# Kernel optimization log

Measured on AMD Instinct MI355X. Metric: run time of the kernel, lower is better.

## Reference

```python
import jax, jax.numpy as jnp
import numpy as np

B, S, E, H, LD, P, NC = 4, 256, 256, 8, 128, 256, 2
N = S * P  # total points (static)
EPS = 1e-5


def setup_inputs() -> dict:
    key = jax.random.key(0)
    ks = jax.random.split(key, 12)
    r = lambda i, shape, s: jax.random.normal(ks[i], shape, jnp.float32) * s
    return dict(
        gl_feats=jax.random.normal(ks[0], (S, B, E), jnp.float32),
        lo_feats=jax.random.normal(ks[1], (B, N, LD), jnp.float32),
        centroids=jax.random.normal(ks[2], (B, S, 2), jnp.float32),
        np_cluster=jnp.full((S,), P, jnp.int32),
        fc1_w=r(3, (16, 2), 0.5), fc1_b=jnp.zeros(16, jnp.float32),
        fc2_w=r(4, (E, 16), 0.1), fc2_b=jnp.zeros(E, jnp.float32),
        in_proj_w=r(5, (3 * E, E), 0.05), in_proj_b=jnp.zeros(3 * E, jnp.float32),
        out_proj_w=r(6, (E, E), 0.05), out_proj_b=jnp.zeros(E, jnp.float32),
        conv2_w=r(7, (E // 2, LD + E), 0.05), conv2_b=jnp.zeros(E // 2, jnp.float32),
        bn2_gamma=jnp.ones(E // 2, jnp.float32), bn2_beta=jnp.zeros(E // 2, jnp.float32),
        bn2_mean=jnp.zeros(E // 2, jnp.float32), bn2_var=jnp.ones(E // 2, jnp.float32),
        conv3_w=r(8, (64, E // 2), 0.05), conv3_b=jnp.zeros(64, jnp.float32),
        bn3_gamma=jnp.ones(64, jnp.float32), bn3_beta=jnp.zeros(64, jnp.float32),
        bn3_mean=jnp.zeros(64, jnp.float32), bn3_var=jnp.ones(64, jnp.float32),
        conv4_w=r(9, (NC, 64), 0.05), conv4_b=jnp.zeros(NC, jnp.float32),
    )


def _bn(z, g, b, m, v):
    # inference-mode BatchNorm1d over the channel (last) axis
    return (z - m) * jax.lax.rsqrt(v + EPS) * g + b


def reference(gl_feats, lo_feats, centroids, np_cluster,
              fc1_w, fc1_b, fc2_w, fc2_b,
              in_proj_w, in_proj_b, out_proj_w, out_proj_b,
              conv2_w, conv2_b, bn2_gamma, bn2_beta, bn2_mean, bn2_var,
              conv3_w, conv3_b, bn3_gamma, bn3_beta, bn3_mean, bn3_var,
              conv4_w, conv4_b):
    # positional encoding of centroids: Linear(2,16) -> leaky_relu -> Linear(16,E)
    h = centroids @ fc1_w.T + fc1_b                      # [B,S,16]
    h = jnp.where(h >= 0, h, 0.01 * h)                   # leaky_relu_, slope 0.01
    pos = h @ fc2_w.T + fc2_b                            # [B,S,E]
    x = gl_feats.transpose(1, 0, 2) + pos                # [B,S,E] (torch MHA is seq-first)

    # MultiheadAttention (self-attn, eval-mode dropout=identity)
    qkv = x @ in_proj_w.T + in_proj_b                    # [B,S,3E]
    q, k, v = jnp.split(qkv, 3, axis=-1)
    dh = E // H
    qh = q.reshape(B, S, H, dh)
    kh = k.reshape(B, S, H, dh)
    vh = v.reshape(B, S, H, dh)
    scores = jnp.einsum('bqhd,bkhd->bhqk', qh, kh) * (1.0 / np.sqrt(dh))
    attn = jax.nn.softmax(scores, axis=-1)               # [B,H,S,S]
    ctx = jnp.einsum('bhqk,bkhd->bqhd', attn, vh).reshape(B, S, E)
    attn_out = ctx @ out_proj_w.T + out_proj_b           # [B,S,E]

    # segment-broadcast: replace the python repeat/cat loop with a gather
    cluster_ids = jnp.repeat(jnp.arange(S), np_cluster, total_repeat_length=N)  # [N]
    global_feat = attn_out[:, cluster_ids, :]            # [B,N,E]

    pc = jnp.concatenate([lo_feats, global_feat], axis=2)  # [B,N,LD+E]
    # 1x1 Conv1d == pointwise Linear over channels
    h2 = jax.nn.relu(_bn(pc @ conv2_w.T + conv2_b, bn2_gamma, bn2_beta, bn2_mean, bn2_var))
    h3 = jax.nn.relu(_bn(h2 @ conv3_w.T + conv3_b, bn3_gamma, bn3_beta, bn3_mean, bn3_var))
    out = h3 @ conv4_w.T + conv4_b                       # [B,N,NC]
    return out.transpose(0, 2, 1)                        # [B,NC,N] to match torch layout
```

## Files before the change

### kernel.cpp

```cpp
#include <hip/hip_runtime.h>

#define B_   4
#define S_   256
#define E_   256
#define H_   8
#define LD_  128
#define N_   65536
#define NC_  2

typedef __attribute__((ext_vector_type(8))) short s8v;
typedef __attribute__((ext_vector_type(4))) float f32x4;

__device__ __forceinline__ short f2bf(float f) {
  union { float f; unsigned u; } v; v.f = f;
  unsigned r = (v.u + 0x7FFFu + ((v.u >> 16) & 1u)) >> 16;
  return (short)r;
}
__device__ __forceinline__ float bf2f(short s) {
  union { float f; unsigned u; } v; v.u = ((unsigned)(unsigned short)s) << 16;
  return v.f;
}
__device__ __forceinline__ s8v pack8(float4 a, float4 b) {
  s8v r;
  r[0] = f2bf(a.x); r[1] = f2bf(a.y); r[2] = f2bf(a.z); r[3] = f2bf(a.w);
  r[4] = f2bf(b.x); r[5] = f2bf(b.y); r[6] = f2bf(b.z); r[7] = f2bf(b.w);
  return r;
}

__global__ __launch_bounds__(256) void ids_pre_k(const int* __restrict__ npc,
                                                 int* __restrict__ pre) {
  __shared__ int ps[257];
  int t = threadIdx.x;
  if (t == 0) {
    ps[0] = 0;
    for (int s = 0; s < 256; s++) ps[s + 1] = ps[s] + npc[s];
  }
  __syncthreads();
  pre[t] = ps[t];
  if (t == 0) pre[256] = ps[256];
}

__global__ __launch_bounds__(256) void ids_fill_k(const int* __restrict__ pre,
                                                  int* __restrict__ ids) {
  int s = blockIdx.x, t = threadIdx.x;
  if (s < 256) {
    int st = pre[s], en = pre[s + 1]; if (en > N_) en = N_;
    for (int n = st + t; n < en; n += 256) ids[n] = s;
  } else {
    int st = pre[256];
    for (int n = st + t; n < N_; n += 256) ids[n] = 255;
  }
}

__global__ __launch_bounds__(256) void cvt_w_k(
    const float* __restrict__ ipw, const float* __restrict__ opw,
    const float* __restrict__ w2, const float* __restrict__ w3,
    const float* __restrict__ b2, const float* __restrict__ g2,
    const float* __restrict__ be2, const float* __restrict__ mu2,
    const float* __restrict__ va2,
    const float* __restrict__ b3, const float* __restrict__ g3,
    const float* __restrict__ be3, const float* __restrict__ mu3,
    const float* __restrict__ va3,
    short* __restrict__ iph, short* __restrict__ ipl,
    short* __restrict__ oph, short* __restrict__ opl,
    short* __restrict__ w2bf, short* __restrict__ w3bf,
    float* __restrict__ sc2, float* __restrict__ sh2,
    float* __restrict__ sc3, float* __restrict__ sh3) {
  int i = blockIdx.x * 256 + threadIdx.x;
  if (i < 196608) {
    float v = ipw[i]; short h = f2bf(v);
    iph[i] = h; ipl[i] = f2bf(v - bf2f(h));
  }
  if (i < 65536) {
    float v = opw[i]; short h = f2bf(v);
    oph[i] = h; opl[i] = f2bf(v - bf2f(h));
  }
  if (i < 49152) w2bf[i] = f2bf(w2[i]);
  if (i < 8192)  w3bf[i] = f2bf(w3[i]);
  if (i < 128) {
    float sc = g2[i] * rsqrtf(va2[i] + 1e-5f);
    sc2[i] = sc; sh2[i] = (b2[i] - mu2[i]) * sc + be2[i];
  }
  if (i < 64) {
    float sc = g3[i] * rsqrtf(va3[i] + 1e-5f);
    sc3[i] = sc; sh3[i] = (b3[i] - mu3[i]) * sc + be3[i];
  }
}

__global__ __launch_bounds__(256) void pos_x_k(const float* __restrict__ gl,
                                               const float* __restrict__ cen,
                                               const float* __restrict__ fc1w,
                                               const float* __restrict__ fc1b,
                                               const float* __restrict__ fc2w,
                                               const float* __restrict__ fc2b,
                                               short* __restrict__ Xhi,
                                               short* __restrict__ Xlo) {
  int bs = blockIdx.x;
  int b = bs >> 8, s = bs & 255;
  __shared__ float hsh[16];
  int t = threadIdx.x;
  if (t < 16) {
    float c0 = cen[bs * 2 + 0], c1 = cen[bs * 2 + 1];
    float v = c0 * fc1w[2 * t] + c1 * fc1w[2 * t + 1] + fc1b[t];
    hsh[t] = (v >= 0.f) ? v : 0.01f * v;
  }
  __syncthreads();
  float p = fc2b[t];
#pragma unroll
  for (int j = 0; j < 16; j++) p += hsh[j] * fc2w[t * 16 + j];
  float v = gl[((size_t)s * B_ + b) * E_ + t] + p;
  short h = f2bf(v);
  Xhi[(size_t)bs * E_ + t] = h;
  Xlo[(size_t)bs * E_ + t] = f2bf(v - bf2f(h));
}

__global__ __launch_bounds__(256) void gemm_x3_k(
    const short* __restrict__ Ah, const short* __restrict__ Al,
    const short* __restrict__ Wh, const short* __restrict__ Wl,
    const float* __restrict__ bias, float* __restrict__ Cf,
    short* __restrict__ Cb, int M, int N, int K) {
  __shared__ __align__(16) short gs[18432];
  const int AH = 0, AL = 4608, WH = 9216, WL = 13824;
  int t = threadIdx.x;
  int row0 = blockIdx.x * 64, col0 = blockIdx.y * 64;
  int w = t >> 6, l = t & 63, quad = l >> 4, lr = l & 15;
  int m0 = w * 16;
  int ar = t >> 2, aq = (t & 3) * 16;
  f32x4 acc[4];
#pragma unroll
  for (int i = 0; i < 4; i++) acc[i] = (f32x4)(0.f);

  for (int kc = 0; kc < K; kc += 64) {
    __syncthreads();
    {
      size_t ra = (size_t)(row0 + ar) * K + kc + aq;
      size_t rw = (size_t)(col0 + ar) * K + kc + aq;
      *(s8v*)&gs[AH + ar * 72 + aq]     = *(const s8v*)&Ah[ra];
      *(s8v*)&gs[AH + ar * 72 + aq + 8] = *(const s8v*)&Ah[ra + 8];
      *(s8v*)&gs[AL + ar * 72 + aq]     = *(const s8v*)&Al[ra];
      *(s8v*)&gs[AL + ar * 72 + aq + 8] = *(const s8v*)&Al[ra + 8];
      *(s8v*)&gs[WH + ar * 72 + aq]     = *(const s8v*)&Wh[rw];
      *(s8v*)&gs[WH + ar * 72 + aq + 8] = *(const s8v*)&Wh[rw + 8];
      *(s8v*)&gs[WL + ar * 72 + aq]     = *(const s8v*)&Wl[rw];
      *(s8v*)&gs[WL + ar * 72 + aq + 8] = *(const s8v*)&Wl[rw + 8];
    }
    __syncthreads();
#pragma unroll
    for (int ks = 0; ks < 2; ks++) {
      int ko = ks * 32 + quad * 8;
      s8v ah = *(const s8v*)&gs[AH + (m0 + lr) * 72 + ko];
      s8v al = *(const s8v*)&gs[AL + (m0 + lr) * 72 + ko];
      s8v bh[4], bl[4];
#pragma unroll
      for (int ct = 0; ct < 4; ct++) {
        bh[ct] = *(const s8v*)&gs[WH + (ct * 16 + lr) * 72 + ko];
        bl[ct] = *(const s8v*)&gs[WL + (ct * 16 + lr) * 72 + ko];
      }
#pragma unroll
      for (int ct = 0; ct < 4; ct++) {
        acc[ct] = __builtin_amdgcn_mfma_f32_16x16x32_bf16(ah, bh[ct], acc[ct], 0, 0, 0);
        acc[ct] = __builtin_amdgcn_mfma_f32_16x16x32_bf16(al, bh[ct], acc[ct], 0, 0, 0);
        acc[ct] = __builtin_amdgcn_mfma_f32_16x16x32_bf16(ah, bl[ct], acc[ct], 0, 0, 0);
      }
    }
  }
#pragma unroll
  for (int ct = 0; ct < 4; ct++) {
    int c = col0 + ct * 16 + lr;
    float bb = bias[c];
#pragma unroll
    for (int rg = 0; rg < 4; rg++) {
      int r = row0 + m0 + quad * 4 + rg;
      float v = acc[ct][rg] + bb;
      if (Cb) Cb[(size_t)r * N + c] = f2bf(v);
      else    Cf[(size_t)r * N + c] = v;
    }
  }
}

__global__ __launch_bounds__(256) void attn_k(const float* __restrict__ qkv,
                                              short* __restrict__ Chi,
                                              short* __restrict__ Clo) {
  int bid = blockIdx.x;
  int qt = bid & 7, h = (bid >> 3) & 7, b = bid >> 6;
  __shared__ __align__(16) float smem[16384];
  float* Kx = smem;
  float* Vx = smem + 8192;
  int t = threadIdx.x;
#pragma unroll
  for (int i = 0; i < 8; i++) {
    int row = i * 32 + (t >> 3);
    int d4 = (t & 7) * 4;
    const float* base = qkv + (size_t)(b * S_ + row) * 768 + h * 32 + d4;
    *(float4*)&Kx[row * 32 + d4] = *(const float4*)(base + 256);
    *(float4*)&Vx[row * 32 + d4] = *(const float4*)(base + 512);
  }
  int r = t & 31, g = t >> 5;
  float q[32];
  {
    const float* qb = qkv + (size_t)(b * S_ + qt * 32 + r) * 768 + h * 32;
#pragma unroll
    for (int d4 = 0; d4 < 32; d4 += 4) {
      float4 v = *(const float4*)(qb + d4);
      q[d4] = v.x; q[d4 + 1] = v.y; q[d4 + 2] = v.z; q[d4 + 3] = v.w;
    }
  }
  __syncthreads();
  const float scale = 0.17677669529663687f;
  int kk0 = g * 32;
  float sc[32];
  float m = -1e30f;
#pragma unroll
  for (int kk = 0; kk < 32; kk++) {
    const float* kr = &Kx[(kk0 + kk) * 32];
    float4 a = (float4){0.f, 0.f, 0.f, 0.f};
#pragma unroll
    for (int d4 = 0; d4 < 32; d4 += 4) {
      float4 kv = *(const float4*)(kr + d4);
      a.x += q[d4] * kv.x; a.y += q[d4 + 1] * kv.y;
      a.z += q[d4 + 2] * kv.z; a.w += q[d4 + 3] * kv.w;
    }
    float s = ((a.x + a.y) + (a.z + a.w)) * scale;
    sc[kk] = s;
    m = fmaxf(m, s);
  }
  float lsum = 0.f;
  float ctx[32];
#pragma unroll
  for (int d = 0; d < 32; d++) ctx[d] = 0.f;
#pragma unroll
  for (int kk = 0; kk < 32; kk++) {
    const float* vr = &Vx[(kk0 + kk) * 32];
    float p = __expf(sc[kk] - m);
    lsum += p;
#pragma unroll
    for (int d4 = 0; d4 < 32; d4 += 4) {
      float4 vv = *(const float4*)(vr + d4);
      ctx[d4] += p * vv.x; ctx[d4 + 1] += p * vv.y;
      ctx[d4 + 2] += p * vv.z; ctx[d4 + 3] += p * vv.w;
    }
  }
  __syncthreads();
  float* ctxbuf = smem;
  float* mbuf = smem + 8192;
  float* lbuf = smem + 8448;
  mbuf[g * 32 + r] = m;
  lbuf[g * 32 + r] = lsum;
#pragma unroll
  for (int d = 0; d < 32; d++)
    ctxbuf[(g * 32 + r) * 32 + ((d + r) & 31)] = ctx[d];
  __syncthreads();
  int r2 = t & 31, dq = t >> 5;
  float M = -1e30f;
#pragma unroll
  for (int gg = 0; gg < 8; gg++) M = fmaxf(M, mbuf[gg * 32 + r2]);
  float wg[8]; float L = 0.f;
#pragma unroll
  for (int gg = 0; gg < 8; gg++) {
    wg[gg] = __expf(mbuf[gg * 32 + r2] - M);
    L += lbuf[gg * 32 + r2] * wg[gg];
  }
  float invL = 1.f / L;
  size_t base = (size_t)(b * S_ + qt * 32 + r2) * E_ + h * 32;
#pragma unroll
  for (int dd = 0; dd < 4; dd++) {
    int d = dq * 4 + dd;
    float o = 0.f;
#pragma unroll
    for (int gg = 0; gg < 8; gg++)
      o += ctxbuf[(gg * 32 + r2) * 32 + ((d + r2) & 31)] * wg[gg];
    o *= invL;
    short hi = f2bf(o);
    Chi[base + d] = hi;
    Clo[base + d] = f2bf(o - bf2f(hi));
  }
}

#define H2O   0
#define SW3O  17408
#define H3O   26112

__global__ __launch_bounds__(256, 2) void conv_fused_k(
    const float* __restrict__ lo, const short* __restrict__ attnb,
    const int* __restrict__ ids,
    const short* __restrict__ w2bf, const short* __restrict__ w3bf,
    const float* __restrict__ sc2, const float* __restrict__ sh2,
    const float* __restrict__ sc3, const float* __restrict__ sh3,
    const float* __restrict__ w4, const float* __restrict__ b4,
    float* __restrict__ out) {
  __shared__ __align__(16) short smem[36864];
  int t = threadIdx.x;
  int bid = blockIdx.x;
  int b = bid >> 9;
  int n0 = (bid & 511) << 7;
  int w = t >> 6, l = t & 63;
  int quad = l >> 4, lr = l & 15;
  int mh = w & 1, chh = w >> 1;

  int ar = t >> 1, akh = (t & 1) * 32;
  int sid = ids[n0 + ar];
  const float* lob = &lo[((size_t)b * N_ + n0 + ar) * LD_ + akh];
  const short* atb = &attnb[((size_t)b * S_ + sid) * E_ + akh];
  const short* wb  = &w2bf[ar * 384 + akh];
  int swr = ar * 72 + akh;

  f32x4 acc2[4][4];
#pragma unroll
  for (int i = 0; i < 4; i++)
#pragma unroll
    for (int j = 0; j < 4; j++) acc2[i][j] = (f32x4)(0.f);

  float4 pf[8]; s8v pa[4]; s8v pw[4];
#pragma unroll
  for (int j = 0; j < 8; j++) pf[j] = *(const float4*)(lob + j * 4);
#pragma unroll
  for (int j = 0; j < 4; j++) pw[j] = *(const s8v*)(wb + j * 8);
#pragma unroll
  for (int j = 0; j < 4; j++)
    *(s8v*)&smem[swr + j * 8] = pack8(pf[2 * j], pf[2 * j + 1]);
#pragma unroll
  for (int j = 0; j < 4; j++) *(s8v*)&smem[18432 + swr + j * 8] = pw[j];
  __syncthreads();

  for (int kc = 0; kc < 6; kc++) {
    int cb = kc & 1;
    int sa_c = cb * 9216, sw_c = 18432 + cb * 9216;
    int sa_n = (cb ^ 1) * 9216, sw_n = 18432 + (cb ^ 1) * 9216;
    int kn = kc + 1;
    if (kn < 6) {
      if (kn < 2) {
#pragma unroll
        for (int j = 0; j < 8; j++) pf[j] = *(const float4*)(lob + kn * 64 + j * 4);
      } else {
#pragma unroll
        for (int j = 0; j < 4; j++) pa[j] = *(const s8v*)(atb + (kn - 2) * 64 + j * 8);
      }
#pragma unroll
      for (int j = 0; j < 4; j++) pw[j] = *(const s8v*)(wb + kn * 64 + j * 8);
    }
#pragma unroll
    for (int ks = 0; ks < 2; ks++) {
      int ko = ks * 32 + quad * 8;
      s8v af[4], bf[4];
#pragma unroll
      for (int mt = 0; mt < 4; mt++)
        af[mt] = *(const s8v*)&smem[sa_c + (64 * mh + 16 * mt + lr) * 72 + ko];
#pragma unroll
      for (int ct = 0; ct < 4; ct++)
        bf[ct] = *(const s8v*)&smem[sw_c + (64 * chh + 16 * ct + lr) * 72 + ko];
#pragma unroll
      for (int mt = 0; mt < 4; mt++)
#pragma unroll
        for (int ct = 0; ct < 4; ct++)
          acc2[mt][ct] = __builtin_amdgcn_mfma_f32_16x16x32_bf16(af[mt], bf[ct], acc2[mt][ct], 0, 0, 0);
    }
    if (kn < 6) {
      if (kn < 2) {
#pragma unroll
        for (int j = 0; j < 4; j++)
          *(s8v*)&smem[sa_n + swr + j * 8] = pack8(pf[2 * j], pf[2 * j + 1]);
      } else {
#pragma unroll
        for (int j = 0; j < 4; j++) *(s8v*)&smem[sa_n + swr + j * 8] = pa[j];
      }
#pragma unroll
      for (int j = 0; j < 4; j++) *(s8v*)&smem[sw_n + swr + j * 8] = pw[j];
    }
    __syncthreads();
  }

#pragma unroll
  for (int ct = 0; ct < 4; ct++) {
    int c = 64 * chh + 16 * ct + lr;
    float sc = sc2[c], sh = sh2[c];
#pragma unroll
    for (int mt = 0; mt < 4; mt++)
#pragma unroll
      for (int rg = 0; rg < 4; rg++) {
        int p = 64 * mh + 16 * mt + 4 * quad + rg;
        float z = acc2[mt][ct][rg] * sc + sh;
        smem[H2O + p * 136 + c] = f2bf(fmaxf(z, 0.f));
      }
  }
  {
    int ch = t >> 2, kq = (t & 3) * 32;
#pragma unroll
    for (int j = 0; j < 4; j++)
      *(s8v*)&smem[SW3O + ch * 136 + kq + j * 8] =
          *(const s8v*)&w3bf[ch * 128 + kq + j * 8];
  }
  __syncthreads();

  f32x4 acc3[2][4];
#pragma unroll
  for (int i = 0; i < 2; i++)
#pragma unroll
    for (int j = 0; j < 4; j++) acc3[i][j] = (f32x4)(0.f);
#pragma unroll
  for (int ks = 0; ks < 4; ks++) {
    int ko = ks * 32 + quad * 8;
    s8v af[2], bf[4];
#pragma unroll
    for (int mt = 0; mt < 2; mt++)
      af[mt] = *(const s8v*)&smem[H2O + (32 * w + 16 * mt + lr) * 136 + ko];
#pragma unroll
    for (int ct = 0; ct < 4; ct++)
      bf[ct] = *(const s8v*)&smem[SW3O + (16 * ct + lr) * 136 + ko];
#pragma unroll
    for (int mt = 0; mt < 2; mt++)
#pragma unroll
      for (int ct = 0; ct < 4; ct++)
        acc3[mt][ct] = __builtin_amdgcn_mfma_f32_16x16x32_bf16(af[mt], bf[ct], acc3[mt][ct], 0, 0, 0);
  }

#pragma unroll
  for (int ct = 0; ct < 4; ct++) {
    int c = 16 * ct + lr;
    float sc = sc3[c], sh = sh3[c];
#pragma unroll
    for (int mt = 0; mt < 2; mt++)
#pragma unroll
      for (int rg = 0; rg < 4; rg++) {
        int p = 32 * w + 16 * mt + 4 * quad + rg;
        float z = acc3[mt][ct][rg] * sc + sh;
        smem[H3O + p * 72 + c] = f2bf(fmaxf(z, 0.f));
      }
  }
  __syncthreads();

  {
    int c = t >> 7, p = t & 127;
    float s = b4[c];
#pragma unroll
    for (int j = 0; j < 8; j++) {
      s8v hv = *(const s8v*)&smem[H3O + p * 72 + j * 8];
#pragma unroll
      for (int e = 0; e < 8; e++)
        s += bf2f(hv[e]) * w4[c * 64 + j * 8 + e];
    }
    out[((size_t)b * NC_ + c) * N_ + n0 + p] = s;
  }
}

extern "C" void kernel_launch(void* const* d_in, const int* in_sizes, int n_in,
                              void* d_out, int out_size, void* d_ws, size_t ws_size,
                              hipStream_t stream) {
  const float* gl   = (const float*)d_in[0];
  const float* lo   = (const float*)d_in[1];
  const float* cen  = (const float*)d_in[2];
  const int*   npc  = (const int*)d_in[3];
  const float* fc1w = (const float*)d_in[4];
  const float* fc1b = (const float*)d_in[5];
  const float* fc2w = (const float*)d_in[6];
  const float* fc2b = (const float*)d_in[7];
  const float* ipw  = (const float*)d_in[8];
  const float* ipb  = (const float*)d_in[9];
  const float* opw  = (const float*)d_in[10];
  const float* opb  = (const float*)d_in[11];
  const float* w2   = (const float*)d_in[12];
  const float* b2   = (const float*)d_in[13];
  const float* g2   = (const float*)d_in[14];
  const float* be2  = (const float*)d_in[15];
  const float* mu2  = (const float*)d_in[16];
  const float* va2  = (const float*)d_in[17];
  const float* w3   = (const float*)d_in[18];
  const float* b3   = (const float*)d_in[19];
  const float* g3   = (const float*)d_in[20];
  const float* be3  = (const float*)d_in[21];
  const float* mu3  = (const float*)d_in[22];
  const float* va3  = (const float*)d_in[23];
  const float* w4   = (const float*)d_in[24];
  const float* b4   = (const float*)d_in[25];

  char* ws = (char*)d_ws;
  float* qkv  = (float*)(ws);
  short* Xhi  = (short*)(ws + 3145728);
  short* Xlo  = (short*)(ws + 3670016);
  short* Chi  = (short*)(ws + 4194304);
  short* Clo  = (short*)(ws + 4718592);
  short* atb  = (short*)(ws + 5242880);
  short* iph  = (short*)(ws + 5767168);
  short* ipl  = (short*)(ws + 6160384);
  short* oph  = (short*)(ws + 6553600);
  short* opl  = (short*)(ws + 6684672);
  short* w2bf = (short*)(ws + 6815744);
  short* w3bf = (short*)(ws + 6914048);
  int*   ids  = (int*)  (ws + 6930432);
  int*   pre  = (int*)  (ws + 7192576);
  float* sc2  = (float*)(ws + 7194624);
  float* sh2  = (float*)(ws + 7195136);
  float* sc3  = (float*)(ws + 7195648);
  float* sh3  = (float*)(ws + 7195904);
  float* out  = (float*)d_out;

  cvt_w_k<<<768, 256, 0, stream>>>(ipw, opw, w2, w3, b2, g2, be2, mu2, va2,
                                   b3, g3, be3, mu3, va3,
                                   iph, ipl, oph, opl, w2bf, w3bf,
                                   sc2, sh2, sc3, sh3);
  ids_pre_k<<<1, 256, 0, stream>>>(npc, pre);
  ids_fill_k<<<257, 256, 0, stream>>>(pre, ids);
  pos_x_k<<<B_ * S_, 256, 0, stream>>>(gl, cen, fc1w, fc1b, fc2w, fc2b, Xhi, Xlo);
  gemm_x3_k<<<dim3(16, 12), 256, 0, stream>>>(Xhi, Xlo, iph, ipl, ipb,
                                              qkv, nullptr, B_ * S_, 768, E_);
  attn_k<<<B_ * H_ * 8, 256, 0, stream>>>(qkv, Chi, Clo);
  gemm_x3_k<<<dim3(16, 4), 256, 0, stream>>>(Chi, Clo, oph, opl, opb,
                                             nullptr, atb, B_ * S_, E_, E_);
  conv_fused_k<<<B_ * (N_ / 128), 256, 0, stream>>>(
      lo, atb, ids, w2bf, w3bf, sc2, sh2, sc3, sh3, w4, b4, out);
}
```

Before: 317.8 us.

## Precompute global-feature conv2 contribution per cluster and merge prep kernels

Splits conv2 into its local part and its global part, which depends only on the cluster. The global part, attn_out @ W2_global^T, is computed once per (batch, cluster) in a new out-proj+conv2 kernel and gathered as a bias in the fused point kernel. This cuts the per-point K dimension from 384 to 128 and removes gathering 256-wide attention rows for every point. The three small prep kernels (weight conversion, cluster-id prefix/fill, positional encoding) are merged into one launch, and conv_fused uses less LDS so three blocks can fit per CU. The out-projection now runs on only 16 blocks, which may serialize, and G is added in fp32 before BN.

```diff
diff --git a/kernel.cpp b/kernel.cpp
--- a/kernel.cpp
+++ b/kernel.cpp
@@ -27,32 +27,8 @@
   return r;
 }
 
-__global__ __launch_bounds__(256) void ids_pre_k(const int* __restrict__ npc,
-                                                 int* __restrict__ pre) {
-  __shared__ int ps[257];
-  int t = threadIdx.x;
-  if (t == 0) {
-    ps[0] = 0;
-    for (int s = 0; s < 256; s++) ps[s + 1] = ps[s] + npc[s];
-  }
-  __syncthreads();
-  pre[t] = ps[t];
-  if (t == 0) pre[256] = ps[256];
-}
-
-__global__ __launch_bounds__(256) void ids_fill_k(const int* __restrict__ pre,
-                                                  int* __restrict__ ids) {
-  int s = blockIdx.x, t = threadIdx.x;
-  if (s < 256) {
-    int st = pre[s], en = pre[s + 1]; if (en > N_) en = N_;
-    for (int n = st + t; n < en; n += 256) ids[n] = s;
-  } else {
-    int st = pre[256];
-    for (int n = st + t; n < N_; n += 256) ids[n] = 255;
-  }
-}
-
-__global__ __launch_bounds__(256) void cvt_w_k(
+__global__ __launch_bounds__(256) void prep_k(
+    const int* __restrict__ npc, int* __restrict__ ids,
     const float* __restrict__ ipw, const float* __restrict__ opw,
     const float* __restrict__ w2, const float* __restrict__ w3,
     const float* __restrict__ b2, const float* __restrict__ g2,
@@ -65,60 +41,74 @@
     short* __restrict__ oph, short* __restrict__ opl,
     short* __restrict__ w2bf, short* __restrict__ w3bf,
     float* __restrict__ sc2, float* __restrict__ sh2,
-    float* __restrict__ sc3, float* __restrict__ sh3) {
-  int i = blockIdx.x * 256 + threadIdx.x;
-  if (i < 196608) {
-    float v = ipw[i]; short h = f2bf(v);
-    iph[i] = h; ipl[i] = f2bf(v - bf2f(h));
-  }
-  if (i < 65536) {
-    float v = opw[i]; short h = f2bf(v);
-    oph[i] = h; opl[i] = f2bf(v - bf2f(h));
-  }
-  if (i < 49152) w2bf[i] = f2bf(w2[i]);
-  if (i < 8192)  w3bf[i] = f2bf(w3[i]);
-  if (i < 128) {
-    float sc = g2[i] * rsqrtf(va2[i] + 1e-5f);
-    sc2[i] = sc; sh2[i] = (b2[i] - mu2[i]) * sc + be2[i];
-  }
-  if (i < 64) {
-    float sc = g3[i] * rsqrtf(va3[i] + 1e-5f);
-    sc3[i] = sc; sh3[i] = (b3[i] - mu3[i]) * sc + be3[i];
-  }
-}
-
-__global__ __launch_bounds__(256) void pos_x_k(const float* __restrict__ gl,
-                                               const float* __restrict__ cen,
-                                               const float* __restrict__ fc1w,
-                                               const float* __restrict__ fc1b,
-                                               const float* __restrict__ fc2w,
-                                               const float* __restrict__ fc2b,
-                                               short* __restrict__ Xhi,
-                                               short* __restrict__ Xlo) {
-  int bs = blockIdx.x;
-  int b = bs >> 8, s = bs & 255;
+    float* __restrict__ sc3, float* __restrict__ sh3,
+    const float* __restrict__ gl, const float* __restrict__ cen,
+    const float* __restrict__ fc1w, const float* __restrict__ fc1b,
+    const float* __restrict__ fc2w, const float* __restrict__ fc2b,
+    short* __restrict__ Xhi, short* __restrict__ Xlo) {
+  __shared__ int red[256];
   __shared__ float hsh[16];
-  int t = threadIdx.x;
-  if (t < 16) {
-    float c0 = cen[bs * 2 + 0], c1 = cen[bs * 2 + 1];
-    float v = c0 * fc1w[2 * t] + c1 * fc1w[2 * t + 1] + fc1b[t];
-    hsh[t] = (v >= 0.f) ? v : 0.01f * v;
-  }
-  __syncthreads();
-  float p = fc2b[t];
-#pragma unroll
-  for (int j = 0; j < 16; j++) p += hsh[j] * fc2w[t * 16 + j];
-  float v = gl[((size_t)s * B_ + b) * E_ + t] + p;
-  short h = f2bf(v);
-  Xhi[(size_t)bs * E_ + t] = h;
-  Xlo[(size_t)bs * E_ + t] = f2bf(v - bf2f(h));
+  int bid = blockIdx.x, t = threadIdx.x;
+  if (bid < 768) {
+    int i = bid * 256 + t;
+    if (i < 196608) {
+      float v = ipw[i]; short h = f2bf(v);
+      iph[i] = h; ipl[i] = f2bf(v - bf2f(h));
+    }
+    if (i < 65536) {
+      float v = opw[i]; short h = f2bf(v);
+      oph[i] = h; opl[i] = f2bf(v - bf2f(h));
+    }
+    if (i < 49152) w2bf[i] = f2bf(w2[i]);
+    if (i < 8192)  w3bf[i] = f2bf(w3[i]);
+    if (i < 128) {
+      float sc = g2[i] * rsqrtf(va2[i] + 1e-5f);
+      sc2[i] = sc; sh2[i] = (b2[i] - mu2[i]) * sc + be2[i];
+    }
+    if (i < 64) {
+      float sc = g3[i] * rsqrtf(va3[i] + 1e-5f);
+      sc3[i] = sc; sh3[i] = (b3[i] - mu3[i]) * sc + be3[i];
+    }
+  } else if (bid <= 1024) {
+    int s = bid - 768;
+    int val = (s == 256) ? npc[t] : ((t < s) ? npc[t] : 0);
+    red[t] = val;
+    __syncthreads();
+    for (int off = 128; off > 0; off >>= 1) {
+      if (t < off) red[t] += red[t + off];
+      __syncthreads();
+    }
+    int st = red[0];
+    if (s < 256) {
+      int en = st + npc[s]; if (en > N_) en = N_;
+      for (int n = st + t; n < en; n += 256) ids[n] = s;
+    } else {
+      for (int n = st + t; n < N_; n += 256) ids[n] = 255;
+    }
+  } else {
+    int bs = bid - 1025;
+    int b = bs >> 8, s = bs & 255;
+    if (t < 16) {
+      float c0 = cen[bs * 2 + 0], c1 = cen[bs * 2 + 1];
+      float v = c0 * fc1w[2 * t] + c1 * fc1w[2 * t + 1] + fc1b[t];
+      hsh[t] = (v >= 0.f) ? v : 0.01f * v;
+    }
+    __syncthreads();
+    float p = fc2b[t];
+#pragma unroll
+    for (int j = 0; j < 16; j++) p += hsh[j] * fc2w[t * 16 + j];
+    float v = gl[((size_t)s * B_ + b) * E_ + t] + p;
+    short h = f2bf(v);
+    Xhi[(size_t)bs * E_ + t] = h;
+    Xlo[(size_t)bs * E_ + t] = f2bf(v - bf2f(h));
+  }
 }
 
 __global__ __launch_bounds__(256) void gemm_x3_k(
     const short* __restrict__ Ah, const short* __restrict__ Al,
     const short* __restrict__ Wh, const short* __restrict__ Wl,
     const float* __restrict__ bias, float* __restrict__ Cf,
-    short* __restrict__ Cb, int M, int N, int K) {
+    int M, int N, int K) {
   __shared__ __align__(16) short gs[18432];
   const int AH = 0, AL = 4608, WH = 9216, WL = 13824;
   int t = threadIdx.x;
@@ -150,17 +140,13 @@
       int ko = ks * 32 + quad * 8;
       s8v ah = *(const s8v*)&gs[AH + (m0 + lr) * 72 + ko];
       s8v al = *(const s8v*)&gs[AL + (m0 + lr) * 72 + ko];
-      s8v bh[4], bl[4];
 #pragma unroll
       for (int ct = 0; ct < 4; ct++) {
-        bh[ct] = *(const s8v*)&gs[WH + (ct * 16 + lr) * 72 + ko];
-        bl[ct] = *(const s8v*)&gs[WL + (ct * 16 + lr) * 72 + ko];
-      }
-#pragma unroll
-      for (int ct = 0; ct < 4; ct++) {
-        acc[ct] = __builtin_amdgcn_mfma_f32_16x16x32_bf16(ah, bh[ct], acc[ct], 0, 0, 0);
-        acc[ct] = __builtin_amdgcn_mfma_f32_16x16x32_bf16(al, bh[ct], acc[ct], 0, 0, 0);
-        acc[ct] = __builtin_amdgcn_mfma_f32_16x16x32_bf16(ah, bl[ct], acc[ct], 0, 0, 0);
+        s8v bh = *(const s8v*)&gs[WH + (ct * 16 + lr) * 72 + ko];
+        s8v bl = *(const s8v*)&gs[WL + (ct * 16 + lr) * 72 + ko];
+        acc[ct] = __builtin_amdgcn_mfma_f32_16x16x32_bf16(ah, bh, acc[ct], 0, 0, 0);
+        acc[ct] = __builtin_amdgcn_mfma_f32_16x16x32_bf16(al, bh, acc[ct], 0, 0, 0);
+        acc[ct] = __builtin_amdgcn_mfma_f32_16x16x32_bf16(ah, bl, acc[ct], 0, 0, 0);
       }
     }
   }
@@ -171,9 +157,7 @@
 #pragma unroll
     for (int rg = 0; rg < 4; rg++) {
       int r = row0 + m0 + quad * 4 + rg;
-      float v = acc[ct][rg] + bb;
-      if (Cb) Cb[(size_t)r * N + c] = f2bf(v);
-      else    Cf[(size_t)r * N + c] = v;
+      Cf[(size_t)r * N + c] = acc[ct][rg] + bb;
     }
   }
 }
@@ -276,19 +260,115 @@
   }
 }
 
-#define H2O   0
-#define SW3O  17408
-#define H3O   26112
-
-__global__ __launch_bounds__(256, 2) void conv_fused_k(
-    const float* __restrict__ lo, const short* __restrict__ attnb,
+__global__ __launch_bounds__(256) void opg_k(
+    const short* __restrict__ Chi, const short* __restrict__ Clo,
+    const short* __restrict__ oph, const short* __restrict__ opl,
+    const float* __restrict__ opb, const short* __restrict__ w2bf,
+    float* __restrict__ G) {
+  __shared__ __align__(16) short gsm[50688];
+  const int AH = 0, AL = 4608, WH = 9216, WL = 27648;
+  const int CT = 0, W2B = 16896;
+  int t = threadIdx.x;
+  int row0 = blockIdx.x * 64;
+  int w = t >> 6, l = t & 63, quad = l >> 4, lr = l & 15;
+
+  f32x4 acc[16];
+#pragma unroll
+  for (int i = 0; i < 16; i++) acc[i] = (f32x4)(0.f);
+
+  for (int kc = 0; kc < 256; kc += 64) {
+    __syncthreads();
+    {
+#pragma unroll
+      for (int j = 0; j < 8; j++) {
+        *(s8v*)&gsm[WH + t * 72 + j * 8] = *(const s8v*)&oph[(size_t)t * 256 + kc + j * 8];
+        *(s8v*)&gsm[WL + t * 72 + j * 8] = *(const s8v*)&opl[(size_t)t * 256 + kc + j * 8];
+      }
+      if (t < 128) {
+        int row = t >> 1, half = (t & 1) * 32;
+        size_t ra = (size_t)(row0 + row) * 256 + kc + half;
+#pragma unroll
+        for (int j = 0; j < 4; j++) {
+          *(s8v*)&gsm[AH + row * 72 + half + j * 8] = *(const s8v*)&Chi[ra + j * 8];
+          *(s8v*)&gsm[AL + row * 72 + half + j * 8] = *(const s8v*)&Clo[ra + j * 8];
+        }
+      }
+    }
+    __syncthreads();
+#pragma unroll
+    for (int ks = 0; ks < 2; ks++) {
+      int ko = ks * 32 + quad * 8;
+      s8v ah = *(const s8v*)&gsm[AH + (w * 16 + lr) * 72 + ko];
+      s8v al = *(const s8v*)&gsm[AL + (w * 16 + lr) * 72 + ko];
+#pragma unroll
+      for (int ct = 0; ct < 16; ct++) {
+        s8v bh = *(const s8v*)&gsm[WH + (ct * 16 + lr) * 72 + ko];
+        s8v bl = *(const s8v*)&gsm[WL + (ct * 16 + lr) * 72 + ko];
+        acc[ct] = __builtin_amdgcn_mfma_f32_16x16x32_bf16(ah, bh, acc[ct], 0, 0, 0);
+        acc[ct] = __builtin_amdgcn_mfma_f32_16x16x32_bf16(al, bh, acc[ct], 0, 0, 0);
+        acc[ct] = __builtin_amdgcn_mfma_f32_16x16x32_bf16(ah, bl, acc[ct], 0, 0, 0);
+      }
+    }
+  }
+  __syncthreads();
+#pragma unroll
+  for (int ct = 0; ct < 16; ct++) {
+    int c = ct * 16 + lr;
+    float bb = opb[c];
+#pragma unroll
+    for (int rg = 0; rg < 4; rg++) {
+      int r = w * 16 + quad * 4 + rg;
+      gsm[CT + r * 264 + c] = f2bf(acc[ct][rg] + bb);
+    }
+  }
+  {
+    int ch = t >> 1, koff = (t & 1) * 128;
+#pragma unroll
+    for (int j = 0; j < 16; j++)
+      *(s8v*)&gsm[W2B + ch * 264 + koff + j * 8] =
+          *(const s8v*)&w2bf[(size_t)ch * 384 + 128 + koff + j * 8];
+  }
+  __syncthreads();
+  f32x4 acc2[8];
+#pragma unroll
+  for (int i = 0; i < 8; i++) acc2[i] = (f32x4)(0.f);
+#pragma unroll
+  for (int ks = 0; ks < 8; ks++) {
+    int ko = ks * 32 + quad * 8;
+    s8v a = *(const s8v*)&gsm[CT + (w * 16 + lr) * 264 + ko];
+#pragma unroll
+    for (int ct = 0; ct < 8; ct++) {
+      s8v b = *(const s8v*)&gsm[W2B + (ct * 16 + lr) * 264 + ko];
+      acc2[ct] = __builtin_amdgcn_mfma_f32_16x16x32_bf16(a, b, acc2[ct], 0, 0, 0);
+    }
+  }
+#pragma unroll
+  for (int ct = 0; ct < 8; ct++) {
+    int c = ct * 16 + lr;
+#pragma unroll
+    for (int rg = 0; rg < 4; rg++) {
+      int r = row0 + w * 16 + quad * 4 + rg;
+      G[(size_t)r * 128 + c] = acc2[ct][rg];
+    }
+  }
+}
+
+#define CF_SW2 0
+#define CF_SA  17408
+#define CF_H2  0
+#define CF_SW3 17408
+#define CF_H3  0
+
+__global__ __launch_bounds__(256, 3) void conv_fused_k(
+    const float* __restrict__ lo, const float* __restrict__ G,
     const int* __restrict__ ids,
     const short* __restrict__ w2bf, const short* __restrict__ w3bf,
     const float* __restrict__ sc2, const float* __restrict__ sh2,
     const float* __restrict__ sc3, const float* __restrict__ sh3,
     const float* __restrict__ w4, const float* __restrict__ b4,
     float* __restrict__ out) {
-  __shared__ __align__(16) short smem[36864];
+  __shared__ __align__(16) short smem[26624];
+  __shared__ int lds_ids[128];
   int t = threadIdx.x;
   int bid = blockIdx.x;
   int b = bid >> 9;
@@ -296,13 +376,27 @@
   int w = t >> 6, l = t & 63;
   int quad = l >> 4, lr = l & 15;
   int mh = w & 1, chh = w >> 1;
-
   int ar = t >> 1, akh = (t & 1) * 32;
-  int sid = ids[n0 + ar];
   const float* lob = &lo[((size_t)b * N_ + n0 + ar) * LD_ + akh];
-  const short* atb = &attnb[((size_t)b * S_ + sid) * E_ + akh];
-  const short* wb  = &w2bf[ar * 384 + akh];
-  int swr = ar * 72 + akh;
+
+  {
+    int ch = t >> 1, koff = (t & 1) * 64;
+#pragma unroll
+    for (int j = 0; j < 8; j++)
+      *(s8v*)&smem[CF_SW2 + ch * 136 + koff + j * 8] =
+          *(const s8v*)&w2bf[(size_t)ch * 384 + koff + j * 8];
+  }
+  if (t < 128) lds_ids[t] = ids[n0 + t];
+  float4 pf[8];
+#pragma unroll
+  for (int j = 0; j < 8; j++) pf[j] = *(const float4*)(lob + j * 4);
+#pragma unroll
+  for (int j = 0; j < 4; j++)
+    *(s8v*)&smem[CF_SA + ar * 72 + akh + j * 8] = pack8(pf[2 * j], pf[2 * j + 1]);
+  __syncthreads();
+
+#pragma unroll
+  for (int j = 0; j < 8; j++) pf[j] = *(const float4*)(lob + 64 + j * 4);
 
   f32x4 acc2[4][4];
 #pragma unroll
@@ -310,83 +404,72 @@
 #pragma unroll
     for (int j = 0; j < 4; j++) acc2[i][j] = (f32x4)(0.f);
 
-  float4 pf[8]; s8v pa[4]; s8v pw[4];
-#pragma unroll
-  for (int j = 0; j < 8; j++) pf[j] = *(const float4*)(lob + j * 4);
-#pragma unroll
-  for (int j = 0; j < 4; j++) pw[j] = *(const s8v*)(wb + j * 8);
+#pragma unroll
+  for (int ks = 0; ks < 2; ks++) {
+    int ko = ks * 32 + quad * 8;
+    s8v af[4], bf[4];
+#pragma unroll
+    for (int mt = 0; mt < 4; mt++)
+      af[mt] = *(const s8v*)&smem[CF_SA + (64 * mh + 16 * mt + lr) * 72 + ko];
+#pragma unroll
+    for (int ct = 0; ct < 4; ct++)
+      bf[ct] = *(const s8v*)&smem[CF_SW2 + (64 * chh + 16 * ct + lr) * 136 + ko];
+#pragma unroll
+    for (int mt = 0; mt < 4; mt++)
+#pragma unroll
+      for (int ct = 0; ct < 4; ct++)
+        acc2[mt][ct] = __builtin_amdgcn_mfma_f32_16x16x32_bf16(af[mt], bf[ct], acc2[mt][ct], 0, 0, 0);
+  }
+  __syncthreads();
 #pragma unroll
   for (int j = 0; j < 4; j++)
-    *(s8v*)&smem[swr + j * 8] = pack8(pf[2 * j], pf[2 * j + 1]);
-#pragma unroll
-  for (int j = 0; j < 4; j++) *(s8v*)&smem[18432 + swr + j * 8] = pw[j];
-  __syncthreads();
-
-  for (int kc = 0; kc < 6; kc++) {
-    int cb = kc & 1;
-    int sa_c = cb * 9216, sw_c = 18432 + cb * 9216;
-    int sa_n = (cb ^ 1) * 9216, sw_n = 18432 + (cb ^ 1) * 9216;
-    int kn = kc + 1;
-    if (kn < 6) {
-      if (kn < 2) {
-#pragma unroll
-        for (int j = 0; j < 8; j++) pf[j] = *(const float4*)(lob + kn * 64 + j * 4);
-      } else {
-#pragma unroll
-        for (int j = 0; j < 4; j++) pa[j] = *(const s8v*)(atb + (kn - 2) * 64 + j * 8);
-      }
-#pragma unroll
-      for (int j = 0; j < 4; j++) pw[j] = *(const s8v*)(wb + kn * 64 + j * 8);
-    }
-#pragma unroll
-    for (int ks = 0; ks < 2; ks++) {
-      int ko = ks * 32 + quad * 8;
-      s8v af[4], bf[4];
-#pragma unroll
-      for (int mt = 0; mt < 4; mt++)
-        af[mt] = *(const s8v*)&smem[sa_c + (64 * mh + 16 * mt + lr) * 72 + ko];
+    *(s8v*)&smem[CF_SA + ar * 72 + akh + j * 8] = pack8(pf[2 * j], pf[2 * j + 1]);
+  __syncthreads();
+#pragma unroll
+  for (int ks = 0; ks < 2; ks++) {
+    int koA = ks * 32 + quad * 8;
+    int koW = 64 + koA;
+    s8v af[4], bf[4];
+#pragma unroll
+    for (int mt = 0; mt < 4; mt++)
+      af[mt] = *(const s8v*)&smem[CF_SA + (64 * mh + 16 * mt + lr) * 72 + koA];
+#pragma unroll
+    for (int ct = 0; ct < 4; ct++)
+      bf[ct] = *(const s8v*)&smem[CF_SW2 + (64 * chh + 16 * ct + lr) * 136 + koW];
+#pragma unroll
+    for (int mt = 0; mt < 4; mt++)
 #pragma unroll
       for (int ct = 0; ct < 4; ct++)
-        bf[ct] = *(const s8v*)&smem[sw_c + (64 * chh + 16 * ct + lr) * 72 + ko];
-#pragma unroll
-      for (int mt = 0; mt < 4; mt++)
-#pragma unroll
-        for (int ct = 0; ct < 4; ct++)
-          acc2[mt][ct] = __builtin_amdgcn_mfma_f32_16x16x32_bf16(af[mt], bf[ct], acc2[mt][ct], 0, 0, 0);
-    }
-    if (kn < 6) {
-      if (kn < 2) {
-#pragma unroll
-        for (int j = 0; j < 4; j++)
-          *(s8v*)&smem[sa_n + swr + j * 8] = pack8(pf[2 * j], pf[2 * j + 1]);
-      } else {
-#pragma unroll
-        for (int j = 0; j < 4; j++) *(s8v*)&smem[sa_n + swr + j * 8] = pa[j];
-      }
-#pragma unroll
-      for (int j = 0; j < 4; j++) *(s8v*)&smem[sw_n + swr + j * 8] = pw[j];
-    }
-    __syncthreads();
-  }
+        acc2[mt][ct] = __builtin_amdgcn_mfma_f32_16x16x32_bf16(af[mt], bf[ct], acc2[mt][ct], 0, 0, 0);
+  }
+  __syncthreads();
 
 #pragma unroll
   for (int ct = 0; ct < 4; ct++) {
     int c = 64 * chh + 16 * ct + lr;
     float sc = sc2[c], sh = sh2[c];
+    float gv[4][4];
 #pragma unroll
     for (int mt = 0; mt < 4; mt++)
 #pragma unroll
       for (int rg = 0; rg < 4; rg++) {
         int p = 64 * mh + 16 * mt + 4 * quad + rg;
-        float z = acc2[mt][ct][rg] * sc + sh;
-        smem[H2O + p * 136 + c] = f2bf(fmaxf(z, 0.f));
+        gv[mt][rg] = G[((size_t)b * 256 + lds_ids[p]) * 128 + c];
+      }
+#pragma unroll
+    for (int mt = 0; mt < 4; mt++)
+#pragma unroll
+      for (int rg = 0; rg < 4; rg++) {
+        int p = 64 * mh + 16 * mt + 4 * quad + rg;
+        float z = (acc2[mt][ct][rg] + gv[mt][rg]) * sc + sh;
+        smem[CF_H2 + p * 136 + c] = f2bf(fmaxf(z, 0.f));
       }
   }
   {
     int ch = t >> 2, kq = (t & 3) * 32;
 #pragma unroll
     for (int j = 0; j < 4; j++)
-      *(s8v*)&smem[SW3O + ch * 136 + kq + j * 8] =
+      *(s8v*)&smem[CF_SW3 + ch * 136 + kq + j * 8] =
           *(const s8v*)&w3bf[ch * 128 + kq + j * 8];
   }
   __syncthreads();
@@ -402,16 +485,17 @@
     s8v af[2], bf[4];
 #pragma unroll
     for (int mt = 0; mt < 2; mt++)
-      af[mt] = *(const s8v*)&smem[H2O + (32 * w + 16 * mt + lr) * 136 + ko];
+      af[mt] = *(const s8v*)&smem[CF_H2 + (32 * w + 16 * mt + lr) * 136 + ko];
 #pragma unroll
     for (int ct = 0; ct < 4; ct++)
-      bf[ct] = *(const s8v*)&smem[SW3O + (16 * ct + lr) * 136 + ko];
+      bf[ct] = *(const s8v*)&smem[CF_SW3 + (16 * ct + lr) * 136 + ko];
 #pragma unroll
     for (int mt = 0; mt < 2; mt++)
 #pragma unroll
       for (int ct = 0; ct < 4; ct++)
         acc3[mt][ct] = __builtin_amdgcn_mfma_f32_16x16x32_bf16(af[mt], bf[ct], acc3[mt][ct], 0, 0, 0);
   }
+  __syncthreads();
 
 #pragma unroll
   for (int ct = 0; ct < 4; ct++) {
@@ -423,7 +507,7 @@
       for (int rg = 0; rg < 4; rg++) {
         int p = 32 * w + 16 * mt + 4 * quad + rg;
         float z = acc3[mt][ct][rg] * sc + sh;
-        smem[H3O + p * 72 + c] = f2bf(fmaxf(z, 0.f));
+        smem[CF_H3 + p * 72 + c] = f2bf(fmaxf(z, 0.f));
       }
   }
   __syncthreads();
@@ -433,7 +517,7 @@
     float s = b4[c];
 #pragma unroll
     for (int j = 0; j < 8; j++) {
-      s8v hv = *(const s8v*)&smem[H3O + p * 72 + j * 8];
+      s8v hv = *(const s8v*)&smem[CF_H3 + p * 72 + j * 8];
 #pragma unroll
       for (int e = 0; e < 8; e++)
         s += bf2f(hv[e]) * w4[c * 64 + j * 8 + e];
@@ -478,7 +562,7 @@
   short* Xlo  = (short*)(ws + 3670016);
   short* Chi  = (short*)(ws + 4194304);
   short* Clo  = (short*)(ws + 4718592);
-  short* atb  = (short*)(ws + 5242880);
+  float* G    = (float*)(ws + 5242880);
   short* iph  = (short*)(ws + 5767168);
   short* ipl  = (short*)(ws + 6160384);
   short* oph  = (short*)(ws + 6553600);
@@ -486,25 +570,22 @@
   short* w2bf = (short*)(ws + 6815744);
   short* w3bf = (short*)(ws + 6914048);
   int*   ids  = (int*)  (ws + 6930432);
-  int*   pre  = (int*)  (ws + 7192576);
-  float* sc2  = (float*)(ws + 7194624);
-  float* sh2  = (float*)(ws + 7195136);
-  float* sc3  = (float*)(ws + 7195648);
-  float* sh3  = (float*)(ws + 7195904);
+  float* sc2  = (float*)(ws + 7192576);
+  float* sh2  = (float*)(ws + 7193088);
+  float* sc3  = (float*)(ws + 7193600);
+  float* sh3  = (float*)(ws + 7193856);
   float* out  = (float*)d_out;
 
-  cvt_w_k<<<768, 256, 0, stream>>>(ipw, opw, w2, w3, b2, g2, be2, mu2, va2,
+  prep_k<<<2049, 256, 0, stream>>>(npc, ids, ipw, opw, w2, w3,
+                                   b2, g2, be2, mu2, va2,
                                    b3, g3, be3, mu3, va3,
                                    iph, ipl, oph, opl, w2bf, w3bf,
-                                   sc2, sh2, sc3, sh3);
-  ids_pre_k<<<1, 256, 0, stream>>>(npc, pre);
-  ids_fill_k<<<257, 256, 0, stream>>>(pre, ids);
-  pos_x_k<<<B_ * S_, 256, 0, stream>>>(gl, cen, fc1w, fc1b, fc2w, fc2b, Xhi, Xlo);
+                                   sc2, sh2, sc3, sh3,
+                                   gl, cen, fc1w, fc1b, fc2w, fc2b, Xhi, Xlo);
   gemm_x3_k<<<dim3(16, 12), 256, 0, stream>>>(Xhi, Xlo, iph, ipl, ipb,
-                                              qkv, nullptr, B_ * S_, 768, E_);
+                                              qkv, B_ * S_, 768, E_);
   attn_k<<<B_ * H_ * 8, 256, 0, stream>>>(qkv, Chi, Clo);
-  gemm_x3_k<<<dim3(16, 4), 256, 0, stream>>>(Chi, Clo, oph, opl, opb,
-                                             nullptr, atb, B_ * S_, E_, E_);
+  opg_k<<<16, 256, 0, stream>>>(Chi, Clo, oph, opl, opb, w2bf, G);
   conv_fused_k<<<B_ * (N_ / 128), 256, 0, stream>>>(
-      lo, atb, ids, w2bf, w3bf, sc2, sh2, sc3, sh3, w4, b4, out);
-}
+      lo, G, ids, w2bf, w3bf, sc2, sh2, sc3, sh3, w4, b4, out);
+}
```

New measurement: 310.4 us. 1.02x faster.
